# Kernel tuning notes

Hardware: AMD Instinct MI355X
Metric: run time of the kernel (lower is better)

The kernel has to match this reference:

```python
import jax, jax.numpy as jnp
import numpy as np

DIM = 256
N_EMBED = 512
B, T = 32, 4096

def setup_inputs() -> dict:
    key = jax.random.key(0)
    k1, k2 = jax.random.split(key)
    return {
        "input": jax.random.normal(k1, (B, T, DIM), dtype=jnp.float32),
        "embedding": jax.random.normal(k2, (N_EMBED, DIM), dtype=jnp.float32),
    }

def reference(input, embedding):
    n_embed, dim = embedding.shape
    # entropy over pairwise distances of L2-normalized codebook rows
    embed_n = embedding / jnp.linalg.norm(embedding, axis=1, keepdims=True)  # [E, D]
    sq = jnp.sum(embed_n * embed_n, axis=1, keepdims=True)                    # [E, 1]
    dist_between = sq - 2.0 * (embed_n @ embed_n.T) + sq.T                    # [E, E]
    entropy = jnp.sum(dist_between)
    # nearest-neighbor assignment against (detached) normalized codebook
    embed_t = jax.lax.stop_gradient(embedding).T                              # [D, E]
    embed_t = embed_t / jnp.linalg.norm(embed_t, axis=0)                      # col-normalized
    flatten = jax.lax.stop_gradient(input.reshape(-1, dim))                   # [N, D]
    dist = (jnp.sum(flatten * flatten, axis=1, keepdims=True)
            - 2.0 * (flatten @ embed_t)
            + jnp.sum(embed_t * embed_t, axis=0, keepdims=True))              # [N, E]
    embed_ind = jnp.argmax(-dist, axis=1)                                     # [N]
    # gather + normalize selected codes (through-gradient to embedding)
    q = embedding[embed_ind]                                                  # [N, D]
    quantize = q / jnp.linalg.norm(q, axis=1, keepdims=True)
    quantize = quantize.reshape(input.shape)
    diff = jnp.mean((quantize - input) ** 2)
    quantize_1 = input + jax.lax.stop_gradient(quantize - input)
    out = (quantize + quantize_1) * 0.5
    loss = diff - (1.0 / n_embed) ** 2 * entropy
    return out, loss, embed_ind
```

## Files before the change

### kernel.cpp

```cpp
#include <hip/hip_runtime.h>
#include <math.h>

#define NROWS  131072
#define OUT_N  33554432
typedef unsigned int uint;

#define WS_DIFF   0
#define C32_OFF   64
#define EHAT_OFF  4096
#define EHATT_OFF (EHAT_OFF + 524288)

__device__ __forceinline__ float f4c(const float4 v, int c) {
    return c == 0 ? v.x : (c == 1 ? v.y : (c == 2 ? v.z : v.w));
}

__device__ __forceinline__ void gl_lds16(const float4* g, float4* l) {
#if __has_builtin(__builtin_amdgcn_global_load_lds)
    __builtin_amdgcn_global_load_lds(
        (const __attribute__((address_space(1))) void*)g,
        (__attribute__((address_space(3))) void*)l, 16, 0, 0);
#else
    *l = *g;
#endif
}

__global__ __launch_bounds__(256) void vq_prep(
    const float* __restrict__ EMB, float* __restrict__ Ehat,
    float* __restrict__ EhatT, float* __restrict__ c32,
    double* __restrict__ diff_sum)
{
    const int tid = threadIdx.x;
    const int tl  = tid & 15;
    const int rG  = tid >> 4;
    const int e   = blockIdx.x * 16 + rG;
    const float* row = EMB + e * 256;

    float v0[8], v1[8];
    #pragma unroll
    for (int j = 0; j < 8; ++j) {
        v0[j] = row[j * 16 + tl];
        v1[j] = row[128 + j * 16 + tl];
    }
    float y0[8], y1[8];
    #pragma unroll
    for (int j = 0; j < 8; ++j) {
        y0[j] = __fmul_rn(v0[j], v0[j]);
        y1[j] = __fmul_rn(v1[j], v1[j]);
    }
    float L0 = __fadd_rn(__fadd_rn(__fadd_rn(y0[0], y0[1]), __fadd_rn(y0[2], y0[3])),
                         __fadd_rn(__fadd_rn(y0[4], y0[5]), __fadd_rn(y0[6], y0[7])));
    float L1 = __fadd_rn(__fadd_rn(__fadd_rn(y1[0], y1[1]), __fadd_rn(y1[2], y1[3])),
                         __fadd_rn(__fadd_rn(y1[4], y1[5]), __fadd_rn(y1[6], y1[7])));
    #pragma unroll
    for (int off = 8; off >= 1; off >>= 1) {
        L0 = __fadd_rn(L0, __shfl_xor(L0, off, 64));
        L1 = __fadd_rn(L1, __shfl_xor(L1, off, 64));
    }
    float ss  = __fadd_rn(L0, L1);
    float nrm = __fsqrt_rn(ss);

    float z0[8], z1[8];
    #pragma unroll
    for (int j = 0; j < 8; ++j) {
        float e0 = __fdiv_rn(v0[j], nrm);
        float e1 = __fdiv_rn(v1[j], nrm);
        Ehat[e * 256 + j * 16 + tl]       = e0;
        Ehat[e * 256 + 128 + j * 16 + tl] = e1;
        EhatT[(j * 16 + tl) * 512 + e]       = e0;
        EhatT[(128 + j * 16 + tl) * 512 + e] = e1;
        z0[j] = __fmul_rn(e0, e0);
        z1[j] = __fmul_rn(e1, e1);
    }
    float T0 = __fadd_rn(__fadd_rn(__fadd_rn(z0[0], z0[1]), __fadd_rn(z0[2], z0[3])),
                         __fadd_rn(__fadd_rn(z0[4], z0[5]), __fadd_rn(z0[6], z0[7])));
    float T1 = __fadd_rn(__fadd_rn(__fadd_rn(z1[0], z1[1]), __fadd_rn(z1[2], z1[3])),
                         __fadd_rn(__fadd_rn(z1[4], z1[5]), __fadd_rn(z1[6], z1[7])));
    #pragma unroll
    for (int off = 8; off >= 1; off >>= 1) {
        T0 = __fadd_rn(T0, __shfl_xor(T0, off, 64));
        T1 = __fadd_rn(T1, __shfl_xor(T1, off, 64));
    }
    if (tl == 0) c32[e] = __fadd_rn(T0, T1);
    if (blockIdx.x == 0 && tid == 0) *diff_sum = 0.0;
}

__global__ __launch_bounds__(256, 2) void vq_main(
    const float* __restrict__ X, const float* __restrict__ EhatT,
    const float* __restrict__ Ehat, const float* __restrict__ C32,
    float* __restrict__ out, float* __restrict__ ind_out,
    double* __restrict__ diff_sum)
{
    __shared__ float4 ET4[32 * 64];
    __shared__ int    indsh[64];
    __shared__ double dred[4];

    const int tid = threadIdx.x;
    const int tj  = tid & 31;
    const int tmG = tid >> 5;
    const int m0  = blockIdx.x * 64;

    const float4* Xb = (const float4*)(X + (size_t)(m0 + tmG * 8) * 256);
    const float4* Ev = (const float4*)EhatT;

    float xxv[8];
    {
        const int tl = tj & 15;
        #pragma unroll
        for (int i = 0; i < 8; ++i) {
            const float* row = X + (size_t)(m0 + tmG * 8 + i) * 256;
            float y0[8], y1[8];
            #pragma unroll
            for (int j = 0; j < 8; ++j) {
                float v0 = row[j * 16 + tl];
                float v1 = row[128 + j * 16 + tl];
                y0[j] = __fmul_rn(v0, v0);
                y1[j] = __fmul_rn(v1, v1);
            }
            float L0 = __fadd_rn(__fadd_rn(__fadd_rn(y0[0], y0[1]), __fadd_rn(y0[2], y0[3])),
                                 __fadd_rn(__fadd_rn(y0[4], y0[5]), __fadd_rn(y0[6], y0[7])));
            float L1 = __fadd_rn(__fadd_rn(__fadd_rn(y1[0], y1[1]), __fadd_rn(y1[2], y1[3])),
                                 __fadd_rn(__fadd_rn(y1[4], y1[5]), __fadd_rn(y1[6], y1[7])));
            #pragma unroll
            for (int off = 8; off >= 1; off >>= 1) {
                L0 = __fadd_rn(L0, __shfl_xor(L0, off, 64));
                L1 = __fadd_rn(L1, __shfl_xor(L1, off, 64));
            }
            xxv[i] = __fadd_rn(L0, L1);
        }
    }

    float bd[8]; int bj[8];
    #pragma unroll
    for (int i = 0; i < 8; ++i) { bd[i] = 3.0e38f; bj[i] = 0; }

    for (int jc = 0; jc < 2; ++jc) {
        float acc[8][8];
        #pragma unroll
        for (int i = 0; i < 8; ++i)
            #pragma unroll
            for (int c = 0; c < 8; ++c) acc[i][c] = 0.0f;

        float4 aN[8];
        #pragma unroll
        for (int i = 0; i < 8; ++i) aN[i] = Xb[i * 64];

        for (int kc = 0; kc < 8; ++kc) {
            __syncthreads();
            #pragma unroll
            for (int p = 0; p < 8; ++p) {
                int L  = p * 256 + tid;
                int kk = L >> 6;
                int j4 = L & 63;
                gl_lds16(&Ev[(size_t)(kc * 32 + kk) * 128 + jc * 64 + j4], &ET4[L]);
            }
            __syncthreads();
            #pragma unroll
            for (int k4 = 0; k4 < 8; ++k4) {
                float4 aC[8];
                #pragma unroll
                for (int i = 0; i < 8; ++i) aC[i] = aN[i];
                const int nf = (k4 < 7) ? (kc * 8 + k4 + 1)
                                        : ((kc < 7) ? (kc + 1) * 8 : 0);
                #pragma unroll
                for (int i = 0; i < 8; ++i) aN[i] = Xb[i * 64 + nf];

                #pragma unroll
                for (int c4 = 0; c4 < 4; ++c4) {
                    const int kb = (k4 * 4 + c4) * 64;
                    float4 b0 = ET4[kb + tj];
                    float4 b1 = ET4[kb + 32 + tj];
                    #pragma unroll
                    for (int i = 0; i < 8; ++i) {
                        float av = f4c(aC[i], c4);
                        acc[i][0] = fmaf(av, b0.x, acc[i][0]);
                        acc[i][1] = fmaf(av, b0.y, acc[i][1]);
                        acc[i][2] = fmaf(av, b0.z, acc[i][2]);
                        acc[i][3] = fmaf(av, b0.w, acc[i][3]);
                        acc[i][4] = fmaf(av, b1.x, acc[i][4]);
                        acc[i][5] = fmaf(av, b1.y, acc[i][5]);
                        acc[i][6] = fmaf(av, b1.z, acc[i][6]);
                        acc[i][7] = fmaf(av, b1.w, acc[i][7]);
                    }
                }
            }
        }
        const float4* C4 = (const float4*)C32;
        float4 cj0 = C4[jc * 64 + tj];
        float4 cj1 = C4[jc * 64 + 32 + tj];
        #pragma unroll
        for (int i = 0; i < 8; ++i) {
            #pragma unroll
            for (int c = 0; c < 4; ++c) {
                float g2  = __fmul_rn(2.0f, acc[i][c]);
                float d32 = __fadd_rn(__fsub_rn(xxv[i], g2), f4c(cj0, c));
                int   j   = jc * 256 + tj * 4 + c;
                if (d32 < bd[i]) { bd[i] = d32; bj[i] = j; }
            }
            #pragma unroll
            for (int c = 0; c < 4; ++c) {
                float g2  = __fmul_rn(2.0f, acc[i][c + 4]);
                float d32 = __fadd_rn(__fsub_rn(xxv[i], g2), f4c(cj1, c));
                int   j   = jc * 256 + 128 + tj * 4 + c;
                if (d32 < bd[i]) { bd[i] = d32; bj[i] = j; }
            }
        }
    }

    #pragma unroll
    for (int off = 1; off <= 16; off <<= 1) {
        #pragma unroll
        for (int i = 0; i < 8; ++i) {
            float od = __shfl_xor(bd[i], off, 64);
            int   oj = __shfl_xor(bj[i], off, 64);
            if (od < bd[i] || (od == bd[i] && oj < bj[i])) { bd[i] = od; bj[i] = oj; }
        }
    }
    if (tj == 0) {
        #pragma unroll
        for (int i = 0; i < 8; ++i) indsh[tmG * 8 + i] = bj[i];
    }

    double dacc = 0.0;
    if (tj == 0) {
        #pragma unroll
        for (int i = 0; i < 8; ++i) dacc += (double)bd[i];
    }
    dacc += __shfl_xor(dacc, 32, 64);
    if ((tid & 63) == 0) dred[tid >> 6] = dacc;
    __syncthreads();
    if (tid == 0) atomicAdd(diff_sum, dred[0] + dred[1] + dred[2] + dred[3]);

    const float4* Eh4 = (const float4*)Ehat;
    float4* out4 = (float4*)out;
    const int cc = tid & 63;
    #pragma unroll
    for (int rr = 0; rr < 64; rr += 4) {
        int row = rr + (tid >> 6);
        int idx = indsh[row];
        out4[(size_t)(m0 + row) * 64 + cc] = Eh4[(size_t)idx * 64 + cc];
    }
    if (tid < 64) ind_out[m0 + tid] = (float)indsh[tid];
}

__global__ __launch_bounds__(256) void vq_ent_fin(
    const float* __restrict__ Ehat, const float* __restrict__ c32,
    const double* __restrict__ diff_sum, float* __restrict__ loss_out)
{
    __shared__ double red[256];
    const int tid = threadIdx.x;
    double sd = 0.0;
    for (int e = 0; e < 512; ++e) sd += (double)Ehat[e * 256 + tid];
    red[tid] = sd * sd;
    __syncthreads();
    for (int st = 128; st; st >>= 1) {
        if (tid < st) red[tid] += red[tid + st];
        __syncthreads();
    }
    double s2 = red[0];
    __syncthreads();
    red[tid] = (double)c32[tid] + (double)c32[tid + 256];
    __syncthreads();
    for (int st = 128; st; st >>= 1) {
        if (tid < st) red[tid] += red[tid + st];
        __syncthreads();
    }
    if (tid == 0) {
        double ent = 2.0 * 512.0 * red[0] - 2.0 * s2;
        *loss_out = (float)((*diff_sum) * (1.0 / (double)OUT_N)
                            - ent * (1.0 / (512.0 * 512.0)));
    }
}

extern "C" void kernel_launch(void* const* d_in, const int* in_sizes, int n_in,
                              void* d_out, int out_size, void* d_ws, size_t ws_size,
                              hipStream_t stream)
{
    const float* X   = (const float*)d_in[0];
    const float* EMB = (const float*)d_in[1];

    float* out      = (float*)d_out;
    float* loss_out = out + OUT_N;
    float* ind_out  = out + OUT_N + 1;

    char* ws = (char*)d_ws;
    double* diff_sum = (double*)(ws + WS_DIFF);
    float*  c32      = (float*) (ws + C32_OFF);
    float*  Ehat     = (float*) (ws + EHAT_OFF);
    float*  EhatT    = (float*) (ws + EHATT_OFF);

    vq_prep<<<32, 256, 0, stream>>>(EMB, Ehat, EhatT, c32, diff_sum);
    vq_main<<<2048, 256, 0, stream>>>(X, EhatT, Ehat, c32, out, ind_out, diff_sum);
    vq_ent_fin<<<1, 256, 0, stream>>>(Ehat, c32, diff_sum, loss_out);
}
```

Baseline: 630.1 us.

## Double-buffer codebook tiles in LDS to overlap loads with FMA compute

The two nested jc/kc loops become one flat loop over 32 half-size tiles of 16 k-rows. Each step prefetches the next tile into the second LDS buffer while it computes on the current one, so only one barrier per step is needed instead of two. The aim is to hide global-to-LDS latency behind the FMA work. In exchange the steps are twice as many with half the work each, and the branchy epilogue inside the loop may add register pressure under launch bounds of 2 blocks.

```diff
diff --git a/kernel.cpp b/kernel.cpp
--- a/kernel.cpp
+++ b/kernel.cpp
@@ -90,7 +90,7 @@
     float* __restrict__ out, float* __restrict__ ind_out,
     double* __restrict__ diff_sum)
 {
-    __shared__ float4 ET4[32 * 64];
+    __shared__ float4 ET4[2][16 * 64];
     __shared__ int    indsh[64];
     __shared__ double dred[4];
 
@@ -133,77 +133,95 @@
     #pragma unroll
     for (int i = 0; i < 8; ++i) { bd[i] = 3.0e38f; bj[i] = 0; }
 
-    for (int jc = 0; jc < 2; ++jc) {
-        float acc[8][8];
-        #pragma unroll
-        for (int i = 0; i < 8; ++i)
-            #pragma unroll
-            for (int c = 0; c < 8; ++c) acc[i][c] = 0.0f;
-
-        float4 aN[8];
-        #pragma unroll
-        for (int i = 0; i < 8; ++i) aN[i] = Xb[i * 64];
-
-        for (int kc = 0; kc < 8; ++kc) {
-            __syncthreads();
-            #pragma unroll
-            for (int p = 0; p < 8; ++p) {
+    #pragma unroll
+    for (int p = 0; p < 4; ++p) {
+        int L = p * 256 + tid;
+        gl_lds16(&Ev[(size_t)(L >> 6) * 128 + (L & 63)], &ET4[0][L]);
+    }
+    float4 aN[8];
+    #pragma unroll
+    for (int i = 0; i < 8; ++i) aN[i] = Xb[i * 64];
+    __syncthreads();
+
+    float acc[8][8];
+    int cur = 0;
+    for (int t = 0; t < 32; ++t) {
+        const int jc = t >> 4;
+        const int kh = t & 15;
+        if (kh == 0) {
+            #pragma unroll
+            for (int i = 0; i < 8; ++i)
+                #pragma unroll
+                for (int c = 0; c < 8; ++c) acc[i][c] = 0.0f;
+        }
+
+        if (t < 31) {
+            const int t1  = t + 1;
+            const int jc1 = t1 >> 4, kh1 = t1 & 15;
+            #pragma unroll
+            for (int p = 0; p < 4; ++p) {
                 int L  = p * 256 + tid;
                 int kk = L >> 6;
                 int j4 = L & 63;
-                gl_lds16(&Ev[(size_t)(kc * 32 + kk) * 128 + jc * 64 + j4], &ET4[L]);
-            }
-            __syncthreads();
-            #pragma unroll
-            for (int k4 = 0; k4 < 8; ++k4) {
-                float4 aC[8];
+                gl_lds16(&Ev[(size_t)(kh1 * 16 + kk) * 128 + jc1 * 64 + j4],
+                         &ET4[cur ^ 1][L]);
+            }
+        }
+
+        #pragma unroll
+        for (int k4 = 0; k4 < 4; ++k4) {
+            float4 aC[8];
+            #pragma unroll
+            for (int i = 0; i < 8; ++i) aC[i] = aN[i];
+            const int nf = (kh * 4 + k4 + 1) & 63;
+            #pragma unroll
+            for (int i = 0; i < 8; ++i) aN[i] = Xb[i * 64 + nf];
+
+            #pragma unroll
+            for (int c4 = 0; c4 < 4; ++c4) {
+                const int kb = (k4 * 4 + c4) * 64;
+                float4 b0 = ET4[cur][kb + tj];
+                float4 b1 = ET4[cur][kb + 32 + tj];
                 #pragma unroll
-                for (int i = 0; i < 8; ++i) aC[i] = aN[i];
-                const int nf = (k4 < 7) ? (kc * 8 + k4 + 1)
-                                        : ((kc < 7) ? (kc + 1) * 8 : 0);
+                for (int i = 0; i < 8; ++i) {
+                    float av = f4c(aC[i], c4);
+                    acc[i][0] = fmaf(av, b0.x, acc[i][0]);
+                    acc[i][1] = fmaf(av, b0.y, acc[i][1]);
+                    acc[i][2] = fmaf(av, b0.z, acc[i][2]);
+                    acc[i][3] = fmaf(av, b0.w, acc[i][3]);
+                    acc[i][4] = fmaf(av, b1.x, acc[i][4]);
+                    acc[i][5] = fmaf(av, b1.y, acc[i][5]);
+                    acc[i][6] = fmaf(av, b1.z, acc[i][6]);
+                    acc[i][7] = fmaf(av, b1.w, acc[i][7]);
+                }
+            }
+        }
+
+        if (kh == 15) {
+            const float4* C4 = (const float4*)C32;
+            float4 cj0 = C4[jc * 64 + tj];
+            float4 cj1 = C4[jc * 64 + 32 + tj];
+            #pragma unroll
+            for (int i = 0; i < 8; ++i) {
                 #pragma unroll
-                for (int i = 0; i < 8; ++i) aN[i] = Xb[i * 64 + nf];
-
+                for (int c = 0; c < 4; ++c) {
+                    float g2  = __fmul_rn(2.0f, acc[i][c]);
+                    float d32 = __fadd_rn(__fsub_rn(xxv[i], g2), f4c(cj0, c));
+                    int   j   = jc * 256 + tj * 4 + c;
+                    if (d32 < bd[i]) { bd[i] = d32; bj[i] = j; }
+                }
                 #pragma unroll
-                for (int c4 = 0; c4 < 4; ++c4) {
-                    const int kb = (k4 * 4 + c4) * 64;
-                    float4 b0 = ET4[kb + tj];
-                    float4 b1 = ET4[kb + 32 + tj];
-                    #pragma unroll
-                    for (int i = 0; i < 8; ++i) {
-                        float av = f4c(aC[i], c4);
-                        acc[i][0] = fmaf(av, b0.x, acc[i][0]);
-                        acc[i][1] = fmaf(av, b0.y, acc[i][1]);
-                        acc[i][2] = fmaf(av, b0.z, acc[i][2]);
-                        acc[i][3] = fmaf(av, b0.w, acc[i][3]);
-                        acc[i][4] = fmaf(av, b1.x, acc[i][4]);
-                        acc[i][5] = fmaf(av, b1.y, acc[i][5]);
-                        acc[i][6] = fmaf(av, b1.z, acc[i][6]);
-                        acc[i][7] = fmaf(av, b1.w, acc[i][7]);
-                    }
+                for (int c = 0; c < 4; ++c) {
+                    float g2  = __fmul_rn(2.0f, acc[i][c + 4]);
+                    float d32 = __fadd_rn(__fsub_rn(xxv[i], g2), f4c(cj1, c));
+                    int   j   = jc * 256 + 128 + tj * 4 + c;
+                    if (d32 < bd[i]) { bd[i] = d32; bj[i] = j; }
                 }
             }
         }
-        const float4* C4 = (const float4*)C32;
-        float4 cj0 = C4[jc * 64 + tj];
-        float4 cj1 = C4[jc * 64 + 32 + tj];
-        #pragma unroll
-        for (int i = 0; i < 8; ++i) {
-            #pragma unroll
-            for (int c = 0; c < 4; ++c) {
-                float g2  = __fmul_rn(2.0f, acc[i][c]);
-                float d32 = __fadd_rn(__fsub_rn(xxv[i], g2), f4c(cj0, c));
-                int   j   = jc * 256 + tj * 4 + c;
-                if (d32 < bd[i]) { bd[i] = d32; bj[i] = j; }
-            }
-            #pragma unroll
-            for (int c = 0; c < 4; ++c) {
-                float g2  = __fmul_rn(2.0f, acc[i][c + 4]);
-                float d32 = __fadd_rn(__fsub_rn(xxv[i], g2), f4c(cj1, c));
-                int   j   = jc * 256 + 128 + tj * 4 + c;
-                if (d32 < bd[i]) { bd[i] = d32; bj[i] = j; }
-            }
-        }
+
+        __syncthreads();
+        cur ^= 1;
     }
 
     #pragma unroll
```

Result: slower. 671.0 us (+6.5%).

## Double-buffer codebook tiles in LDS to overlap loads with FMA compute

Applied to the files above, without the earlier changes.

Replaces the single 32-row LDS tile, loaded and consumed between two barriers, with two 16-row ping-pong buffers. The next tile's global-to-LDS copy is issued before computing on the current one, so one barrier per half-step replaces two per chunk. The aim is to hide global load latency behind the FMA work. LDS use stays the same, but the flattened loop adds control flow and more barrier points.

```diff
diff --git a/kernel.cpp b/kernel.cpp
--- a/kernel.cpp
+++ b/kernel.cpp
@@ -84,13 +84,80 @@
     if (blockIdx.x == 0 && tid == 0) *diff_sum = 0.0;
 }
 
+#define STAGE_T(T1, ETBUF) do {                                               \
+    const int jc1_ = (T1) >> 4, kh1_ = (T1) & 15;                             \
+    _Pragma("unroll")                                                         \
+    for (int p_ = 0; p_ < 4; ++p_) {                                          \
+        int L_  = p_ * 256 + tid;                                             \
+        int kk_ = L_ >> 6;                                                    \
+        int j4_ = L_ & 63;                                                    \
+        gl_lds16(&Ev[(size_t)(kh1_ * 16 + kk_) * 128 + jc1_ * 64 + j4_],      \
+                 &ETBUF[L_]);                                                 \
+    }                                                                         \
+} while (0)
+
+#define COMPUTE_T(KH, ETBUF) do {                                             \
+    const int fb_ = (KH) * 4;                                                 \
+    _Pragma("unroll")                                                         \
+    for (int k4 = 0; k4 < 4; ++k4) {                                          \
+        float4 aC[8];                                                         \
+        _Pragma("unroll")                                                     \
+        for (int i = 0; i < 8; ++i) aC[i] = aN[i];                            \
+        const int nf_ = (k4 == 3) ? ((fb_ + 4) & 63) : (fb_ + k4 + 1);        \
+        _Pragma("unroll")                                                     \
+        for (int i = 0; i < 8; ++i) aN[i] = Xb[i * 64 + nf_];                 \
+        _Pragma("unroll")                                                     \
+        for (int c4 = 0; c4 < 4; ++c4) {                                      \
+            const int kb = (k4 * 4 + c4) * 64;                                \
+            float4 b0 = ETBUF[kb + tj];                                       \
+            float4 b1 = ETBUF[kb + 32 + tj];                                  \
+            _Pragma("unroll")                                                 \
+            for (int i = 0; i < 8; ++i) {                                     \
+                float av = f4c(aC[i], c4);                                    \
+                acc[i][0] = fmaf(av, b0.x, acc[i][0]);                        \
+                acc[i][1] = fmaf(av, b0.y, acc[i][1]);                        \
+                acc[i][2] = fmaf(av, b0.z, acc[i][2]);                        \
+                acc[i][3] = fmaf(av, b0.w, acc[i][3]);                        \
+                acc[i][4] = fmaf(av, b1.x, acc[i][4]);                        \
+                acc[i][5] = fmaf(av, b1.y, acc[i][5]);                        \
+                acc[i][6] = fmaf(av, b1.z, acc[i][6]);                        \
+                acc[i][7] = fmaf(av, b1.w, acc[i][7]);                        \
+            }                                                                 \
+        }                                                                     \
+    }                                                                         \
+} while (0)
+
+#define EPI_T(JC) do {                                                        \
+    const float4* C4_ = (const float4*)C32;                                   \
+    float4 cj0 = C4_[(JC) * 64 + tj];                                         \
+    float4 cj1 = C4_[(JC) * 64 + 32 + tj];                                    \
+    _Pragma("unroll")                                                         \
+    for (int i = 0; i < 8; ++i) {                                             \
+        _Pragma("unroll")                                                     \
+        for (int c = 0; c < 4; ++c) {                                         \
+            float g2  = __fmul_rn(2.0f, acc[i][c]);                           \
+            float d32 = __fadd_rn(__fsub_rn(xxv[i], g2), f4c(cj0, c));        \
+            int   j   = (JC) * 256 + tj * 4 + c;                              \
+            if (d32 < bd[i]) { bd[i] = d32; bj[i] = j; }                      \
+        }                                                                     \
+        _Pragma("unroll")                                                     \
+        for (int c = 0; c < 4; ++c) {                                         \
+            float g2  = __fmul_rn(2.0f, acc[i][c + 4]);                       \
+            float d32 = __fadd_rn(__fsub_rn(xxv[i], g2), f4c(cj1, c));        \
+            int   j   = (JC) * 256 + 128 + tj * 4 + c;                        \
+            if (d32 < bd[i]) { bd[i] = d32; bj[i] = j; }                      \
+        }                                                                     \
+    }                                                                         \
+} while (0)
+
 __global__ __launch_bounds__(256, 2) void vq_main(
     const float* __restrict__ X, const float* __restrict__ EhatT,
     const float* __restrict__ Ehat, const float* __restrict__ C32,
     float* __restrict__ out, float* __restrict__ ind_out,
     double* __restrict__ diff_sum)
 {
-    __shared__ float4 ET4[32 * 64];
+    __shared__ float4 ET_A[16 * 64];
+    __shared__ float4 ET_B[16 * 64];
     __shared__ int    indsh[64];
     __shared__ double dred[4];
 
@@ -133,77 +200,32 @@
     #pragma unroll
     for (int i = 0; i < 8; ++i) { bd[i] = 3.0e38f; bj[i] = 0; }
 
-    for (int jc = 0; jc < 2; ++jc) {
-        float acc[8][8];
-        #pragma unroll
-        for (int i = 0; i < 8; ++i)
+    STAGE_T(0, ET_A);
+    float4 aN[8];
+    #pragma unroll
+    for (int i = 0; i < 8; ++i) aN[i] = Xb[i * 64];
+    float acc[8][8];
+    __syncthreads();
+
+    #pragma unroll 1
+    for (int tp = 0; tp < 16; ++tp) {
+        const int tA = tp * 2;
+        const int tB = tA + 1;
+
+        if ((tA & 15) == 0) {
             #pragma unroll
-            for (int c = 0; c < 8; ++c) acc[i][c] = 0.0f;
-
-        float4 aN[8];
-        #pragma unroll
-        for (int i = 0; i < 8; ++i) aN[i] = Xb[i * 64];
-
-        for (int kc = 0; kc < 8; ++kc) {
-            __syncthreads();
-            #pragma unroll
-            for (int p = 0; p < 8; ++p) {
-                int L  = p * 256 + tid;
-                int kk = L >> 6;
-                int j4 = L & 63;
-                gl_lds16(&Ev[(size_t)(kc * 32 + kk) * 128 + jc * 64 + j4], &ET4[L]);
-            }
-            __syncthreads();
-            #pragma unroll
-            for (int k4 = 0; k4 < 8; ++k4) {
-                float4 aC[8];
+            for (int i = 0; i < 8; ++i)
                 #pragma unroll
-                for (int i = 0; i < 8; ++i) aC[i] = aN[i];
-                const int nf = (k4 < 7) ? (kc * 8 + k4 + 1)
-                                        : ((kc < 7) ? (kc + 1) * 8 : 0);
-                #pragma unroll
-                for (int i = 0; i < 8; ++i) aN[i] = Xb[i * 64 + nf];
-
-                #pragma unroll
-                for (int c4 = 0; c4 < 4; ++c4) {
-                    const int kb = (k4 * 4 + c4) * 64;
-                    float4 b0 = ET4[kb + tj];
-                    float4 b1 = ET4[kb + 32 + tj];
-                    #pragma unroll
-                    for (int i = 0; i < 8; ++i) {
-                        float av = f4c(aC[i], c4);
-                        acc[i][0] = fmaf(av, b0.x, acc[i][0]);
-                        acc[i][1] = fmaf(av, b0.y, acc[i][1]);
-                        acc[i][2] = fmaf(av, b0.z, acc[i][2]);
-                        acc[i][3] = fmaf(av, b0.w, acc[i][3]);
-                        acc[i][4] = fmaf(av, b1.x, acc[i][4]);
-                        acc[i][5] = fmaf(av, b1.y, acc[i][5]);
-                        acc[i][6] = fmaf(av, b1.z, acc[i][6]);
-                        acc[i][7] = fmaf(av, b1.w, acc[i][7]);
-                    }
-                }
-            }
+                for (int c = 0; c < 8; ++c) acc[i][c] = 0.0f;
         }
-        const float4* C4 = (const float4*)C32;
-        float4 cj0 = C4[jc * 64 + tj];
-        float4 cj1 = C4[jc * 64 + 32 + tj];
-        #pragma unroll
-        for (int i = 0; i < 8; ++i) {
-            #pragma unroll
-            for (int c = 0; c < 4; ++c) {
-                float g2  = __fmul_rn(2.0f, acc[i][c]);
-                float d32 = __fadd_rn(__fsub_rn(xxv[i], g2), f4c(cj0, c));
-                int   j   = jc * 256 + tj * 4 + c;
-                if (d32 < bd[i]) { bd[i] = d32; bj[i] = j; }
-            }
-            #pragma unroll
-            for (int c = 0; c < 4; ++c) {
-                float g2  = __fmul_rn(2.0f, acc[i][c + 4]);
-                float d32 = __fadd_rn(__fsub_rn(xxv[i], g2), f4c(cj1, c));
-                int   j   = jc * 256 + 128 + tj * 4 + c;
-                if (d32 < bd[i]) { bd[i] = d32; bj[i] = j; }
-            }
-        }
+        STAGE_T(tB, ET_B);
+        COMPUTE_T(tA & 15, ET_A);
+        __syncthreads();
+
+        if (tp < 15) STAGE_T(tB + 1, ET_A);
+        COMPUTE_T(tB & 15, ET_B);
+        if ((tB & 15) == 15) EPI_T(tB >> 4);
+        __syncthreads();
     }
 
     #pragma unroll
```

After: 2.061 ms. 227% more time.
